# Kernel tuning notes

Measured on AMD Instinct MI355X. Metric: run time of the kernel, lower is better.

The kernel has to match this reference:

```python
import jax, jax.numpy as jnp
import numpy as np

N, C = 262144, 128

def setup_inputs() -> dict:
    key = jax.random.key(0)
    k1, k2 = jax.random.split(key)
    x = jax.random.normal(k1, (N, C), dtype=jnp.float32)
    # binary label matrix (0/1 floats), as implied by the _target[i][0]==0 check
    target = jax.random.randint(k2, (N, C), 0, 2).astype(jnp.float32)
    return {"x": x, "target": target}

def reference(x, target):
    # Per-row argmax over classes (torch.max(_input[i], 0) -> idx)
    idx = jnp.argmax(x, axis=1)                      # [N]
    # Rows where idx > 0 and target[i,0] == 0 get all non-idx target entries zeroed
    cond = (idx > 0) & (target[:, 0] == 0)           # [N]
    keep = jax.nn.one_hot(idx, x.shape[1], dtype=target.dtype)  # [N, C]
    t = jnp.where(cond[:, None], target * keep, target)
    return jnp.mean(jnp.abs(x * t))
```

## Files before the change

kernel.cpp:

```cpp
#include <hip/hip_runtime.h>

#define NROWS 262144
#define NCOLS 128
#define TPB 256
#define WPB (TPB / 64)
#define NBLOCKS (NROWS / TPB)

typedef float floatx4 __attribute__((ext_vector_type(4)));

__global__ __launch_bounds__(TPB) void biased_loss_rows(
    const float* __restrict__ x, const float* __restrict__ t,
    float* __restrict__ partial)
{
    const int row = blockIdx.x * TPB + threadIdx.x;
    const float* xr = x + (size_t)row * NCOLS;
    const float* tr = t + (size_t)row * NCOLS;

    floatx4 xc = *(const floatx4*)xr;
    floatx4 tc = *(const floatx4*)tr;
    const float x0 = xc.x;
    const float t0 = tc.x;

    float M  = xc.x;
    float tM = tc.x;
    float S  = fabsf(xc.x * tc.x);

#define STEP(v, tv)                                   \
    do {                                              \
        if ((v) > M) tM = (tv);      \
        M = fmaxf(M, (v));           \
        S += fabsf((v) * (tv));                       \
    } while (0)

    STEP(xc.y, tc.y);
    STEP(xc.z, tc.z);
    STEP(xc.w, tc.w);

    #pragma unroll
    for (int j = 1; j < NCOLS / 4; ++j) {
        xc = *(const floatx4*)(xr + j * 4);
        tc = *(const floatx4*)(tr + j * 4);
        STEP(xc.x, tc.x);
        STEP(xc.y, tc.y);
        STEP(xc.z, tc.z);
        STEP(xc.w, tc.w);
    }
#undef STEP

    const bool cond = (x0 != M) && (t0 == 0.0f);
    float acc = cond ? fabsf(M) * tM : S;

    #pragma unroll
    for (int off = 32; off > 0; off >>= 1)
        acc += __shfl_xor(acc, off, 64);

    const int lane = threadIdx.x & 63;
    const int waveInBlock = threadIdx.x >> 6;
    __shared__ float smem[WPB];
    if (lane == 0) smem[waveInBlock] = acc;
    __syncthreads();
    if (threadIdx.x == 0) {
        float bsum = 0.0f;
        #pragma unroll
        for (int w = 0; w < WPB; ++w) bsum += smem[w];
        partial[blockIdx.x] = bsum;
    }
}

__global__ __launch_bounds__(256) void reduce_partials(
    const float* __restrict__ partial, float* __restrict__ out, int n)
{
    float acc = 0.0f;
    for (int i = threadIdx.x; i < n; i += 256) acc += partial[i];
    #pragma unroll
    for (int off = 32; off > 0; off >>= 1)
        acc += __shfl_xor(acc, off, 64);
    __shared__ float smem[4];
    const int lane = threadIdx.x & 63, w = threadIdx.x >> 6;
    if (lane == 0) smem[w] = acc;
    __syncthreads();
    if (threadIdx.x == 0) {
        float s = smem[0] + smem[1] + smem[2] + smem[3];
        out[0] = s / (float)((size_t)NROWS * (size_t)NCOLS);
    }
}

extern "C" void kernel_launch(void* const* d_in, const int* in_sizes, int n_in,
                              void* d_out, int out_size, void* d_ws, size_t ws_size,
                              hipStream_t stream) {
    const float* x = (const float*)d_in[0];
    const float* t = (const float*)d_in[1];
    float* partial = (float*)d_ws;

    biased_loss_rows<<<NBLOCKS, TPB, 0, stream>>>(x, t, partial);
    reduce_partials<<<1, 256, 0, stream>>>(partial, (float*)d_out, NBLOCKS);
}
```

Measured before the change: 281.3 us.

## Stage row tiles in LDS via direct global-to-LDS loads with 8 threads per row

Replaces the one-thread-per-row kernel, whose per-thread strided 512-byte row reads are uncoalesced, with blocks that pull 32 rows of x and target into LDS using global_load_lds 16-byte transfers that are fully coalesced per wave. Each row is then processed by 8 threads with a rotated chunk order to reduce LDS bank conflicts, and a shuffle-based argmax reduction breaks ties on the lowest index. The cost is more blocks, LDS usage of 32 KB per block limiting occupancy, and an explicit wait on the loads with no overlap between loading and compute.

```diff
diff --git a/kernel.cpp b/kernel.cpp
--- a/kernel.cpp
+++ b/kernel.cpp
@@ -4,65 +4,97 @@
 #define NCOLS 128
 #define TPB 256
 #define WPB (TPB / 64)
-#define NBLOCKS (NROWS / TPB)
+#define ROWS_PER_BLOCK 32
+#define NBLOCKS (NROWS / ROWS_PER_BLOCK)
+#define ROWS_PER_WAVE 8
 
 typedef float floatx4 __attribute__((ext_vector_type(4)));
 
-__global__ __launch_bounds__(TPB) void biased_loss_rows(
+__global__ __launch_bounds__(TPB) void biased_loss_lds(
     const float* __restrict__ x, const float* __restrict__ t,
     float* __restrict__ partial)
 {
-    const int row = blockIdx.x * TPB + threadIdx.x;
-    const float* xr = x + (size_t)row * NCOLS;
-    const float* tr = t + (size_t)row * NCOLS;
+    __shared__ float lx[ROWS_PER_BLOCK * NCOLS];
+    __shared__ float lt[ROWS_PER_BLOCK * NCOLS];
 
-    floatx4 xc = *(const floatx4*)xr;
-    floatx4 tc = *(const floatx4*)tr;
-    const float x0 = xc.x;
-    const float t0 = tc.x;
+    const int tid  = threadIdx.x;
+    const int lane = tid & 63;
+    const int w    = tid >> 6;
 
-    float M  = xc.x;
-    float tM = tc.x;
-    float S  = fabsf(xc.x * tc.x);
+    const size_t blockRow = (size_t)blockIdx.x * ROWS_PER_BLOCK;
+    #pragma unroll
+    for (int j = 0; j < 4; ++j) {
+        const int lr = w * ROWS_PER_WAVE + 2 * j;
+        const size_t g = (blockRow + lr) * NCOLS + (size_t)lane * 4;
+        __builtin_amdgcn_global_load_lds(
+            (const __attribute__((address_space(1))) void*)(x + g),
+            (__attribute__((address_space(3))) void*)(lx + lr * NCOLS),
+            16, 0, 0);
+        __builtin_amdgcn_global_load_lds(
+            (const __attribute__((address_space(1))) void*)(t + g),
+            (__attribute__((address_space(3))) void*)(lt + lr * NCOLS),
+            16, 0, 0);
+    }
+    asm volatile("s_waitcnt vmcnt(0)" ::: "memory");
+    __builtin_amdgcn_sched_barrier(0);
 
-#define STEP(v, tv)                                   \
-    do {                                              \
-        if ((v) > M) tM = (tv);      \
-        M = fmaxf(M, (v));           \
-        S += fabsf((v) * (tv));                       \
-    } while (0)
+    const int rlocal = tid >> 3;
+    const int q      = tid & 7;
+    const float* lxr = lx + rlocal * NCOLS + q * 16;
+    const float* ltr = lt + rlocal * NCOLS + q * 16;
+    const int rot = rlocal & 3;
 
-    STEP(xc.y, tc.y);
-    STEP(xc.z, tc.z);
-    STEP(xc.w, tc.w);
+    float M = 0.0f, tM = 0.0f, S = 0.0f, t0loc = 0.0f;
+    int jfirst = 0;
 
     #pragma unroll
-    for (int j = 1; j < NCOLS / 4; ++j) {
-        xc = *(const floatx4*)(xr + j * 4);
-        tc = *(const floatx4*)(tr + j * 4);
-        STEP(xc.x, tc.x);
-        STEP(xc.y, tc.y);
-        STEP(xc.z, tc.z);
-        STEP(xc.w, tc.w);
+    for (int k = 0; k < 4; ++k) {
+        const int c = (k + rot) & 3;
+        const floatx4 xc = *(const floatx4*)(lxr + c * 4);
+        const floatx4 tc = *(const floatx4*)(ltr + c * 4);
+
+        float mc = xc.x; int jc = 0; float tmc = tc.x;
+        if (xc.y > mc) { mc = xc.y; jc = 1; tmc = tc.y; }
+        if (xc.z > mc) { mc = xc.z; jc = 2; tmc = tc.z; }
+        if (xc.w > mc) { mc = xc.w; jc = 3; tmc = tc.w; }
+        const int jabs = q * 16 + c * 4 + jc;
+
+        if (k == 0) { M = mc; jfirst = jabs; tM = tmc; }
+        else if (mc > M || (mc == M && jabs < jfirst)) {
+            M = mc; jfirst = jabs; tM = tmc;
+        }
+        if (c == 0) t0loc = tc.x;
+
+        S += fabsf(xc.x * tc.x) + fabsf(xc.y * tc.y)
+           + fabsf(xc.z * tc.z) + fabsf(xc.w * tc.w);
     }
-#undef STEP
 
-    const bool cond = (x0 != M) && (t0 == 0.0f);
-    float acc = cond ? fabsf(M) * tM : S;
+    #pragma unroll
+    for (int off = 1; off <= 4; off <<= 1) {
+        const float oM  = __shfl_xor(M, off, 64);
+        const int   oj  = __shfl_xor(jfirst, off, 64);
+        const float otM = __shfl_xor(tM, off, 64);
+        if (oM > M || (oM == M && oj < jfirst)) { M = oM; jfirst = oj; tM = otM; }
+        S += __shfl_xor(S, off, 64);
+    }
+
+    float acc = 0.0f;
+    if (q == 0) {
+        const bool cond = (jfirst > 0) && (t0loc == 0.0f);
+        acc = cond ? fabsf(M) * tM : S;
+    }
 
     #pragma unroll
     for (int off = 32; off > 0; off >>= 1)
         acc += __shfl_xor(acc, off, 64);
 
-    const int lane = threadIdx.x & 63;
-    const int waveInBlock = threadIdx.x >> 6;
     __shared__ float smem[WPB];
-    if (lane == 0) smem[waveInBlock] = acc;
+    if (lane == 0) smem[w] = acc;
     __syncthreads();
-    if (threadIdx.x == 0) {
+    if (tid == 0) {
         float bsum = 0.0f;
         #pragma unroll
-        for (int w = 0; w < WPB; ++w) bsum += smem[w];
+        for (int i = 0; i < WPB; ++i) bsum += smem[i];
         partial[blockIdx.x] = bsum;
     }
 }
@@ -92,6 +124,6 @@
     const float* t = (const float*)d_in[1];
     float* partial = (float*)d_ws;
 
-    biased_loss_rows<<<NBLOCKS, TPB, 0, stream>>>(x, t, partial);
+    biased_loss_lds<<<NBLOCKS, TPB, 0, stream>>>(x, t, partial);
     reduce_partials<<<1, 256, 0, stream>>>(partial, (float*)d_out, NBLOCKS);
 }
```

Measured after the change: 277.3 us. No clear change (-1.4%).
